# Performance work log

Hardware: AMD Instinct MI355X
Metric: run time of the kernel (lower is better)

Reference implementation:

```python
import jax, jax.numpy as jnp
import numpy as np

NUM_CAPSULE = 32
DIM_CAPSULE = 64
ROUTINGS = 3
EPS = 1e-12  # tf.math.l2_normalize epsilon


def setup_inputs() -> dict:
    key = jax.random.key(0)
    k1, k2 = jax.random.split(key)
    x = jax.random.normal(k1, (32, 2048, 1024), dtype=jnp.float32)
    # shared-weight capsule kernel: (input_dim, num_capsule*dim_capsule), conv1d with kernel size 1
    W = jax.random.normal(k2, (1024, NUM_CAPSULE * DIM_CAPSULE), dtype=jnp.float32) * 0.02
    return {"x": x, "W": W}


def _l2_normalize(v, axis=-1):
    sq = jnp.sum(v * v, axis=axis, keepdims=True)
    return v * jax.lax.rsqrt(jnp.maximum(sq, EPS))


def reference(x, W):
    B, T, _ = x.shape
    # conv1d with kernel size 1 == per-token matmul
    u_hat = jnp.einsum('bti,io->bto', x, W)
    u_hat = u_hat.reshape(B, T, NUM_CAPSULE, DIM_CAPSULE).transpose(0, 2, 1, 3)  # (B, nc, T, dc)
    routing_weights = jnp.zeros((B, NUM_CAPSULE, T), dtype=u_hat.dtype)
    outputs = None
    for i in range(ROUTINGS):
        cw = jax.nn.softmax(routing_weights, axis=1)          # softmax over capsule axis
        # K.batch_dot(cw, u_hat, [2,2]) -> (B,nc,nc,dc), then sum over axis 1
        # == contract sum_i cw[b,i,k] with u_hat[b,j,k,d]
        s = jnp.sum(cw, axis=1)                               # (B, T)
        outputs = jnp.einsum('bk,bjkd->bjd', s, u_hat)        # (B, nc, dc)
        if i < ROUTINGS - 1:
            outputs = _l2_normalize(outputs, axis=-1)
            # K.batch_dot(outputs, u_hat, [2,3]) -> (B,nc,nc,T), then sum over axis 1
            o = jnp.sum(outputs, axis=1)                      # (B, dc)
            routing_weights = jnp.einsum('bd,bjkd->bjk', o, u_hat)  # (B, nc, T)
    return outputs  # activation is linear (None)
```

## Files before the change

### kernel.cpp

```cpp
#include <hip/hip_runtime.h>


#define BATCH   32
#define TLEN    2048
#define DIN     1024
#define DOUT    2048
#define NCHUNK  64
#define RPC     (TLEN / NCHUNK)

__global__ __launch_bounds__(256) void colsum_partial(
    const float* __restrict__ x, float* __restrict__ part)
{
    const int chunk = blockIdx.x;
    const int b     = blockIdx.y;
    const int tx    = threadIdx.x;

    const float4* base = reinterpret_cast<const float4*>(
        x + (size_t)b * TLEN * DIN + (size_t)chunk * RPC * DIN) + tx;

    float4 a0 = make_float4(0.f, 0.f, 0.f, 0.f);
    float4 a1 = make_float4(0.f, 0.f, 0.f, 0.f);
#pragma unroll 8
    for (int r = 0; r < RPC; r += 2) {
        float4 v0 = base[(size_t)r       * (DIN / 4)];
        float4 v1 = base[(size_t)(r + 1) * (DIN / 4)];
        a0.x += v0.x; a0.y += v0.y; a0.z += v0.z; a0.w += v0.w;
        a1.x += v1.x; a1.y += v1.y; a1.z += v1.z; a1.w += v1.w;
    }
    a0.x += a1.x; a0.y += a1.y; a0.z += a1.z; a0.w += a1.w;

    reinterpret_cast<float4*>(part + ((size_t)chunk * BATCH + b) * DIN)[tx] = a0;
}

__global__ __launch_bounds__(256) void chunk_reduce(
    const float* __restrict__ part, float* __restrict__ xs)
{
    const int seg = blockIdx.x;
    const int b   = blockIdx.y;
    const int i   = seg * 256 + threadIdx.x;

    float acc = 0.f;
#pragma unroll 8
    for (int c = 0; c < NCHUNK; ++c)
        acc += part[((size_t)c * BATCH + b) * DIN + i];
    xs[(size_t)b * DIN + i] = acc;
}

#define K3_CB 64
#define K3_BG 4
#define K3_IL (DIN / 4)

__global__ __launch_bounds__(64) void matmul_small(
    const float* __restrict__ xs, const float* __restrict__ W,
    float* __restrict__ out)
{
    const int cb = blockIdx.x;
    const int bg = blockIdx.y;
    const int iq = blockIdx.z;
    const int ol = threadIdx.x;
    const int o  = cb * K3_CB + ol;
    const int i0 = iq * K3_IL;

    const float* wp = W + (size_t)i0 * DOUT + o;
    const float* x0 = xs + (size_t)(bg * K3_BG + 0) * DIN + i0;
    const float* x1 = xs + (size_t)(bg * K3_BG + 1) * DIN + i0;
    const float* x2 = xs + (size_t)(bg * K3_BG + 2) * DIN + i0;
    const float* x3 = xs + (size_t)(bg * K3_BG + 3) * DIN + i0;

    float a0 = 0.f, a1 = 0.f, a2 = 0.f, a3 = 0.f;
#pragma unroll 8
    for (int k = 0; k < K3_IL; ++k) {
        const float w = wp[(size_t)k * DOUT];
        a0 += x0[k] * w;
        a1 += x1[k] * w;
        a2 += x2[k] * w;
        a3 += x3[k] * w;
    }
    atomicAdd(&out[(size_t)(bg * K3_BG + 0) * DOUT + o], a0);
    atomicAdd(&out[(size_t)(bg * K3_BG + 1) * DOUT + o], a1);
    atomicAdd(&out[(size_t)(bg * K3_BG + 2) * DOUT + o], a2);
    atomicAdd(&out[(size_t)(bg * K3_BG + 3) * DOUT + o], a3);
}

extern "C" void kernel_launch(void* const* d_in, const int* in_sizes, int n_in,
                              void* d_out, int out_size, void* d_ws, size_t ws_size,
                              hipStream_t stream)
{
    const float* x = (const float*)d_in[0];
    const float* W = (const float*)d_in[1];
    float* out  = (float*)d_out;
    float* part = (float*)d_ws;
    float* xs   = (float*)d_ws + (size_t)NCHUNK * BATCH * DIN;

    hipMemsetAsync(out, 0, (size_t)BATCH * DOUT * sizeof(float), stream);

    dim3 g1(NCHUNK, BATCH);
    colsum_partial<<<g1, 256, 0, stream>>>(x, part);

    dim3 g2(DIN / 256, BATCH);
    chunk_reduce<<<g2, 256, 0, stream>>>(part, xs);

    dim3 g3(DOUT / K3_CB, BATCH / K3_BG, 4);
    matmul_small<<<g3, 64, 0, stream>>>(xs, W, out);
}
```

Baseline: 74.63 us.

## Fuse chunk reduction into matmul kernel and drop memset and atomics

Merges the chunk-partial reduction and the small matmul into one 1024-thread kernel. Each block reduces the partial column sums for four batches into shared memory, then computes a 256-column output tile with the K split across four thread groups, combined through shared memory. This removes two launches, the memset, the global round-trip of xs and the atomics. The cost is a grid of only 64 blocks, so each block re-reads the partials for its batch group and the W stream is spread across fewer CUs, which may lower the bandwidth available to the matmul.

```diff
diff --git a/kernel.cpp b/kernel.cpp
--- a/kernel.cpp
+++ b/kernel.cpp
@@ -7,6 +7,8 @@
 #define DOUT    2048
 #define NCHUNK  64
 #define RPC     (TLEN / NCHUNK)
+
+typedef float fv4 __attribute__((ext_vector_type(4)));
 
 __global__ __launch_bounds__(256) void colsum_partial(
     const float* __restrict__ x, float* __restrict__ part)
@@ -32,54 +34,60 @@
     reinterpret_cast<float4*>(part + ((size_t)chunk * BATCH + b) * DIN)[tx] = a0;
 }
 
-__global__ __launch_bounds__(256) void chunk_reduce(
-    const float* __restrict__ part, float* __restrict__ xs)
-{
-    const int seg = blockIdx.x;
-    const int b   = blockIdx.y;
-    const int i   = seg * 256 + threadIdx.x;
+#define CBW 256
+#define BGW 4
 
-    float acc = 0.f;
-#pragma unroll 8
-    for (int c = 0; c < NCHUNK; ++c)
-        acc += part[((size_t)c * BATCH + b) * DIN + i];
-    xs[(size_t)b * DIN + i] = acc;
-}
-
-#define K3_CB 64
-#define K3_BG 4
-#define K3_IL (DIN / 4)
-
-__global__ __launch_bounds__(64) void matmul_small(
-    const float* __restrict__ xs, const float* __restrict__ W,
+__global__ __launch_bounds__(1024) void reduce_matmul(
+    const float* __restrict__ part, const float* __restrict__ W,
     float* __restrict__ out)
 {
-    const int cb = blockIdx.x;
-    const int bg = blockIdx.y;
-    const int iq = blockIdx.z;
-    const int ol = threadIdx.x;
-    const int o  = cb * K3_CB + ol;
-    const int i0 = iq * K3_IL;
+    __shared__ float xls[BGW][DIN];
+    __shared__ float ps[4][BGW][CBW];
+
+    const int bid = blockIdx.x;
+    const int cb  = bid & 7;
+    const int bg  = bid >> 3;
+    const int tx  = threadIdx.x;
+
+    {
+        const int i4 = tx & 255;
+        const int bb = tx >> 8;
+        const int b  = bg * BGW + bb;
+        const fv4* pp = reinterpret_cast<const fv4*>(part + (size_t)b * DIN) + i4;
+
+        fv4 acc = {0.f, 0.f, 0.f, 0.f};
+#pragma unroll 8
+        for (int c = 0; c < NCHUNK; ++c)
+            acc += pp[(size_t)c * BATCH * (DIN / 4)];
+        reinterpret_cast<fv4*>(&xls[bb][0])[i4] = acc;
+    }
+    __syncthreads();
+
+    const int ol  = tx & 255;
+    const int iqq = tx >> 8;
+    const int o   = cb * CBW + ol;
+    const int i0  = iqq * 256;
 
     const float* wp = W + (size_t)i0 * DOUT + o;
-    const float* x0 = xs + (size_t)(bg * K3_BG + 0) * DIN + i0;
-    const float* x1 = xs + (size_t)(bg * K3_BG + 1) * DIN + i0;
-    const float* x2 = xs + (size_t)(bg * K3_BG + 2) * DIN + i0;
-    const float* x3 = xs + (size_t)(bg * K3_BG + 3) * DIN + i0;
-
     float a0 = 0.f, a1 = 0.f, a2 = 0.f, a3 = 0.f;
 #pragma unroll 8
-    for (int k = 0; k < K3_IL; ++k) {
+    for (int k = 0; k < 256; ++k) {
         const float w = wp[(size_t)k * DOUT];
-        a0 += x0[k] * w;
-        a1 += x1[k] * w;
-        a2 += x2[k] * w;
-        a3 += x3[k] * w;
+        const int i = i0 + k;
+        a0 += xls[0][i] * w;
+        a1 += xls[1][i] * w;
+        a2 += xls[2][i] * w;
+        a3 += xls[3][i] * w;
     }
-    atomicAdd(&out[(size_t)(bg * K3_BG + 0) * DOUT + o], a0);
-    atomicAdd(&out[(size_t)(bg * K3_BG + 1) * DOUT + o], a1);
-    atomicAdd(&out[(size_t)(bg * K3_BG + 2) * DOUT + o], a2);
-    atomicAdd(&out[(size_t)(bg * K3_BG + 3) * DOUT + o], a3);
+    ps[iqq][0][ol] = a0;
+    ps[iqq][1][ol] = a1;
+    ps[iqq][2][ol] = a2;
+    ps[iqq][3][ol] = a3;
+    __syncthreads();
+
+    const int bb2 = tx >> 8;
+    float s = ps[0][bb2][ol] + ps[1][bb2][ol] + ps[2][bb2][ol] + ps[3][bb2][ol];
+    out[(size_t)(bg * BGW + bb2) * DOUT + o] = s;
 }
 
 extern "C" void kernel_launch(void* const* d_in, const int* in_sizes, int n_in,
@@ -90,16 +98,9 @@
     const float* W = (const float*)d_in[1];
     float* out  = (float*)d_out;
     float* part = (float*)d_ws;
-    float* xs   = (float*)d_ws + (size_t)NCHUNK * BATCH * DIN;
-
-    hipMemsetAsync(out, 0, (size_t)BATCH * DOUT * sizeof(float), stream);
 
     dim3 g1(NCHUNK, BATCH);
     colsum_partial<<<g1, 256, 0, stream>>>(x, part);
 
-    dim3 g2(DIN / 256, BATCH);
-    chunk_reduce<<<g2, 256, 0, stream>>>(part, xs);
-
-    dim3 g3(DOUT / K3_CB, BATCH / K3_BG, 4);
-    matmul_small<<<g3, 64, 0, stream>>>(xs, W, out);
+    reduce_matmul<<<64, 1024, 0, stream>>>(part, W, out);
 }
```

Result: slower. 80.40 us (+7.7%).
